# Kernel optimization log

Measured on AMD Instinct MI355X. Metric: run time of the kernel, lower is better.

## Reference

```python
import jax, jax.numpy as jnp
import numpy as np

IN_DIM, UNITS, OUT_DIM = 128, 256, 8
DENSITY = 0.5  # 1 - sparsity_level
B, T = 256, 512


def _ncp_dims():
    Nm = OUT_DIM
    Nc = max(int(0.4 * (UNITS - Nm)), 1)   # command neurons (AutoNCP rule)
    Ni = UNITS - Nm - Nc                    # inter neurons
    return Ni, Nc, Nm


def _fanout_mask(rng, n_src, n_dst, fanout):
    # each source connects to `fanout` distinct random destinations
    idx = np.argsort(rng.random((n_src, n_dst)), axis=1)[:, :fanout]
    m = np.zeros((n_src, n_dst), dtype=np.int32)
    m[np.arange(n_src)[:, None], idx] = 1
    return m


def setup_inputs() -> dict:
    key = jax.random.key(0)
    rng = np.random.default_rng(22222)
    Ni, Nc, Nm = _ncp_dims()
    s_fan = max(int(Ni * DENSITY), 1)       # sensory fanout
    i_fan = max(int(Nc * DENSITY), 1)       # inter fanout
    m_fanin = max(int(Nc * DENSITY), 1)     # motor fanin
    M_si = _fanout_mask(rng, IN_DIM, Ni, s_fan)      # sensory -> inter
    M_ic = _fanout_mask(rng, Ni, Nc, i_fan)          # inter -> command
    M_cm = _fanout_mask(rng, Nm, Nc, m_fanin).T      # command -> motor (fanin per motor)

    def layer_mask(M_in, hid):
        # WiredCfCCell: concat input sparsity with dense ones for the recurrent block, then transpose
        return np.concatenate([M_in, np.ones((hid, hid), np.int32)], axis=0).T

    masks = [layer_mask(M_si, Ni), layer_mask(M_ic, Nc), layer_mask(M_cm, Nm)]
    dims = [(IN_DIM, Ni), (Ni, Nc), (Nc, Nm)]
    inp = {}
    for l, (fin, hid) in enumerate(dims):
        cat = fin + hid
        scale = 1.0 / np.sqrt(cat)
        for nm in ("w1", "w2", "wa", "wb"):
            inp[f"{nm}_{l}"] = jnp.asarray(rng.normal(0.0, scale, (hid, cat)).astype(np.float32))
        for nm in ("b1", "b2", "ba", "bb"):
            inp[f"{nm}_{l}"] = jnp.zeros((hid,), jnp.float32)
        inp[f"m{l}"] = jnp.asarray(masks[l])  # int32, constant sparsity mask
    k1, k2 = jax.random.split(key)
    inp["x"] = jax.random.normal(k1, (B, T, IN_DIM), jnp.float32)
    inp["dt"] = jax.random.uniform(k2, (1,), jnp.float32, 0.5, 1.5)
    return inp


def _cfc_cell(xh, w1, b1, w2, b2, wa, ba, wb, bb, m, ts):
    # CfCCell, mode='default', no backbone, sparsity mask on ff1/ff2 weights
    mf = m.astype(w1.dtype)
    ff1 = jnp.tanh(xh @ (w1 * mf).T + b1)
    ff2 = jnp.tanh(xh @ (w2 * mf).T + b2)
    t_interp = jax.nn.sigmoid((xh @ wa.T + ba) * ts + (xh @ wb.T + bb))
    return ff1 * (1.0 - t_interp) + t_interp * ff2


def _forward(x, dt, params, masks):
    Ni, Nc, Nm = _ncp_dims()
    ts = dt[0]
    h0 = jnp.zeros((x.shape[0], Ni), x.dtype)
    h1 = jnp.zeros((x.shape[0], Nc), x.dtype)
    h2 = jnp.zeros((x.shape[0], Nm), x.dtype)
    p0, p1, p2 = params

    def step(carry, xt):
        h0, h1, h2 = carry
        nh0 = _cfc_cell(jnp.concatenate([xt, h0], 1), *p0, masks[0], ts)
        nh1 = _cfc_cell(jnp.concatenate([nh0, h1], 1), *p1, masks[1], ts)
        nh2 = _cfc_cell(jnp.concatenate([nh1, h2], 1), *p2, masks[2], ts)
        return (nh0, nh1, nh2), nh2

    (h0, h1, h2), ys = jax.lax.scan(step, (h0, h1, h2), jnp.swapaxes(x, 0, 1))
    y = jnp.tanh(jnp.swapaxes(ys, 0, 1))          # (B, T, OUT_DIM), tanh output saturation
    h_out = jnp.concatenate([h0, h1, h2], axis=1)  # (B, units)
    return y, h_out


def reference(x, dt,
              w1_0, b1_0, w2_0, b2_0, wa_0, ba_0, wb_0, bb_0, m0,
              w1_1, b1_1, w2_1, b2_1, wa_1, ba_1, wb_1, bb_1, m1,
              w1_2, b1_2, w2_2, b2_2, wa_2, ba_2, wb_2, bb_2, m2):
    params = ((w1_0, b1_0, w2_0, b2_0, wa_0, ba_0, wb_0, bb_0),
              (w1_1, b1_1, w2_1, b2_1, wa_1, ba_1, wb_1, bb_1),
              (w1_2, b1_2, w2_2, b2_2, wa_2, ba_2, wb_2, bb_2))
    return _forward(x, dt, params, (m0, m1, m2))
```

## Files before the change

### kernel.cpp

```cpp
#include <hip/hip_runtime.h>
#include <cmath>


typedef _Float16 f16;
typedef f16 h4 __attribute__((ext_vector_type(4)));
typedef f16 h8 __attribute__((ext_vector_type(8)));
typedef float f4 __attribute__((ext_vector_type(4)));

#define MFMA(a, b, c) __builtin_amdgcn_mfma_f32_16x16x32_f16(a, b, c, 0, 0, 0)
#define RAW_BAR() asm volatile("s_waitcnt lgkmcnt(0)\n\ts_barrier" ::: "memory")

constexpr int IN_DIM = 128, Ni = 149, Nc = 99, Nm = 8;
constexpr int CAT0 = 277, CAT1 = 248, CAT2 = 107;
constexpr int Bsz = 256, Tsz = 512;
constexpr int TC = 128, NCH = 4, NBT = 16;
constexpr int NT0 = 30, NT1 = 21;
constexpr int S0 = 168, S2 = 136;
constexpr size_t XU0_HALVES = (size_t)TC * NBT * NT0 * 256;
constexpr size_t NH0_HALVES = (size_t)TC * NBT * 16 * 160;
constexpr size_t XU1_HALVES = (size_t)TC * NBT * NT1 * 256;
constexpr size_t H0S_HALVES = (size_t)NBT * 16 * S0;
constexpr size_t H12S_HALVES = (size_t)NBT * 2 * 16 * S2;
constexpr size_t YOFF = (size_t)Bsz * Tsz * 8;

constexpr int OFF_X0 = 0;
constexpr int OFF_R0 = 7680;
constexpr int OFF_X1 = 17280;
constexpr int OFF_R12A = 24000;
constexpr int OFF_R12B = 29376;
constexpr int NFRAG = 30144;

__device__ inline float rcpf_(float x) { return __builtin_amdgcn_rcpf(x); }
__device__ __forceinline__ float cfc_h(float a0, float a1, float a2) {
  float e0 = __expf(a0), e1 = __expf(a1), e2 = __expf(a2);
  float pa = 1.f + e0, ma = 1.f - e0;
  float pb = 1.f + e1, mb = 1.f - e1;
  float pc = 1.f + e2;
  float num = fmaf(ma * pb, e2, mb * pa);
  return num * rcpf_(pa * pb * pc);
}
__device__ __forceinline__ float tanhp_(float x) {
  float e = __expf(-2.f * x);
  return (1.f - e) * rcpf_(1.f + e);
}

__global__ __launch_bounds__(256) void pack_kernel(
    const float* __restrict__ w1_0, const float* __restrict__ w2_0,
    const float* __restrict__ wa_0, const float* __restrict__ wb_0,
    const int* __restrict__ m0,
    const float* __restrict__ w1_1, const float* __restrict__ w2_1,
    const float* __restrict__ wa_1, const float* __restrict__ wb_1,
    const int* __restrict__ m1,
    const float* __restrict__ w1_2, const float* __restrict__ w2_2,
    const float* __restrict__ wa_2, const float* __restrict__ wb_2,
    const int* __restrict__ m2, const float* __restrict__ dtp,
    f16* __restrict__ PK) {
  int idx = blockIdx.x * 256 + threadIdx.x;
  if (idx >= NFRAG) return;
  int lane = idx & 63, col = lane & 15, q = lane >> 4;
  float ts = dtp[0];
  const float* Wa = nullptr;
  const float* Wb = nullptr;
  const int* M = nullptr;
  int ld, n, nmax, k0, kmax;
  int mat;
  if (idx < OFF_R0) {
    int p = idx >> 6;
    mat = p / 40; int nt = (p >> 2) % 10, kt = p & 3;
    ld = CAT0; n = nt * 16 + col; nmax = Ni; k0 = kt * 32 + q * 8; kmax = IN_DIM;
    if (mat == 0) { Wa = w1_0; M = m0; }
    else if (mat == 1) { Wa = w2_0; M = m0; }
    else { Wa = wa_0; Wb = wb_0; }
  } else if (idx < OFF_X1) {
    int p = (idx - OFF_R0) >> 6;
    int g = p / 15; mat = (p / 5) % 3; int kt = p % 5;
    ld = CAT0; n = g * 16 + col; nmax = Ni; k0 = IN_DIM + kt * 32 + q * 8; kmax = CAT0;
    if (mat == 0) Wa = w1_0;
    else if (mat == 1) Wa = w2_0;
    else { Wa = wa_0; Wb = wb_0; }
  } else if (idx < OFF_R12A) {
    int p = (idx - OFF_X1) >> 6;
    mat = p / 35; int nt = (p / 5) % 7, kt = p % 5;
    ld = CAT1; n = nt * 16 + col; nmax = Nc; k0 = kt * 32 + q * 8; kmax = Ni;
    if (mat == 0) { Wa = w1_1; M = m1; }
    else if (mat == 1) { Wa = w2_1; M = m1; }
    else { Wa = wa_1; Wb = wb_1; }
  } else if (idx < OFF_R12B) {
    int p = (idx - OFF_R12A) >> 6;
    int wv = p / 12; mat = (p / 4) % 3; int kt = p & 3;
    ld = CAT1; n = wv * 16 + col; nmax = Nc; k0 = Ni + kt * 32 + q * 8; kmax = CAT1;
    if (mat == 0) Wa = w1_1;
    else if (mat == 1) Wa = w2_1;
    else { Wa = wa_1; Wb = wb_1; }
  } else {
    int p = (idx - OFF_R12B) >> 6;
    mat = p / 4; int kt = p & 3;
    ld = CAT2; n = col; nmax = Nm; k0 = kt * 32 + q * 8; kmax = CAT2;
    if (mat == 0) { Wa = w1_2; M = m2; }
    else if (mat == 1) { Wa = w2_2; M = m2; }
    else { Wa = wa_2; Wb = wb_2; }
  }
  h8 r;
#pragma unroll
  for (int j = 0; j < 8; j++) {
    int k = k0 + j;
    float v = 0.f;
    if (n < nmax && k < kmax) {
      if (mat < 2) {
        v = Wa[(size_t)n * ld + k];
        if (M) v *= (float)M[(size_t)n * ld + k];
        v *= -2.f;
      } else {
        v = -(ts * Wa[(size_t)n * ld + k] + Wb[(size_t)n * ld + k]);
      }
    }
    r[j] = (f16)v;
  }
  ((h8*)PK)[idx] = r;
}

__global__ __launch_bounds__(192, 2) void X_kernel(
    const h8* __restrict__ pk, const float* __restrict__ x,
    const f16* __restrict__ NH0, f16* __restrict__ XU0, f16* __restrict__ XU1,
    const float* __restrict__ b1_0, const float* __restrict__ b2_0,
    const float* __restrict__ ba_0, const float* __restrict__ bb_0,
    const float* __restrict__ b1_1, const float* __restrict__ b2_1,
    const float* __restrict__ ba_1, const float* __restrict__ bb_1,
    const float* __restrict__ dtp, int c) {
  __shared__ f16 stg[16 * 136];
  int tid = threadIdx.x;
  int w = tid >> 6, lane = tid & 63, col = lane & 15, q = lane >> 4;
  int wg = blockIdx.x;
  float ts = dtp[0];
  if (wg < 512) {
    if (c < 0) return;
    h8 Bf[7][5];
    float bias[7];
#pragma unroll
    for (int nt = 0; nt < 7; nt++) {
#pragma unroll
      for (int kt = 0; kt < 5; kt++)
        Bf[nt][kt] = pk[OFF_X1 + ((w * 7 + nt) * 5 + kt) * 64 + lane];
      int n = nt * 16 + col;
      bias[nt] = (n < Nc) ? (w == 0 ? -2.f * b1_1[n]
                                    : (w == 1 ? -2.f * b2_1[n]
                                              : -(ts * ba_1[n] + bb_1[n])))
                          : 0.f;
    }
    for (int i = 0; i < 4; i++) {
      int mt = wg * 4 + i;
      const f16* Ab = NH0 + (size_t)mt * 2560;
      h8 A[5];
#pragma unroll
      for (int kt = 0; kt < 5; kt++)
        A[kt] = *(const h8*)(Ab + col * 160 + kt * 32 + q * 8);
#pragma unroll
      for (int nt = 0; nt < 7; nt++) {
        float b = bias[nt];
        f4 acc = {b, b, b, b};
#pragma unroll
        for (int kt = 0; kt < 5; kt++) acc = MFMA(A[kt], Bf[nt][kt], acc);
        h4 o;
#pragma unroll
        for (int rr = 0; rr < 4; rr++) o[rr] = (f16)acc[rr];
        *(h4*)(XU1 + ((size_t)mt * NT1 + w * 7 + nt) * 256 + lane * 4) = o;
      }
    }
  } else {
    int cn = c + 1;
    if (cn >= NCH) return;
    int bx = wg - 512;
    h8 Bf[10][4];
    float bias[10];
#pragma unroll
    for (int nt = 0; nt < 10; nt++) {
#pragma unroll
      for (int kt = 0; kt < 4; kt++)
        Bf[nt][kt] = pk[OFF_X0 + ((w * 10 + nt) * 4 + kt) * 64 + lane];
      int n = nt * 16 + col;
      bias[nt] = (n < Ni) ? (w == 0 ? -2.f * b1_0[n]
                                    : (w == 1 ? -2.f * b2_0[n]
                                              : -(ts * ba_0[n] + bb_0[n])))
                          : 0.f;
    }
    for (int i = 0; i < 4; i++) {
      int mt = bx * 4 + i;
      int tl = mt >> 4, bt = mt & 15;
      int tg = cn * TC + tl;
      if (tid < 128) {
        int sr = tid >> 3, sc = (tid & 7) * 16;
        const float* xp = x + ((size_t)(bt * 16 + sr) * Tsz + tg) * IN_DIM + sc;
        h8 hv0, hv1;
#pragma unroll
        for (int j = 0; j < 8; j++) hv0[j] = (f16)xp[j];
#pragma unroll
        for (int j = 0; j < 8; j++) hv1[j] = (f16)xp[8 + j];
        *(h8*)(stg + sr * 136 + sc) = hv0;
        *(h8*)(stg + sr * 136 + sc + 8) = hv1;
      }
      __syncthreads();
      h8 A[4];
#pragma unroll
      for (int kt = 0; kt < 4; kt++)
        A[kt] = *(const h8*)(stg + col * 136 + kt * 32 + q * 8);
#pragma unroll
      for (int nt = 0; nt < 10; nt++) {
        float b = bias[nt];
        f4 acc = {b, b, b, b};
#pragma unroll
        for (int kt = 0; kt < 4; kt++) acc = MFMA(A[kt], Bf[nt][kt], acc);
        h4 o;
#pragma unroll
        for (int rr = 0; rr < 4; rr++) o[rr] = (f16)acc[rr];
        *(h4*)(XU0 + ((size_t)mt * NT0 + w * 10 + nt) * 256 + lane * 4) = o;
      }
      __syncthreads();
    }
  }
}

__device__ __forceinline__ void r0_step(
    const f16* br, f16* bw, const f16* __restrict__ XU0, f16* __restrict__ NH0,
    float* __restrict__ out, const h8 (&Bf)[3][5], h4 (&xu)[3],
    int t, int tload, int bt, int g, int lane, int col, int q, int n, bool last) {
  h8 A[5];
#pragma unroll
  for (int kt = 0; kt < 5; kt++)
    A[kt] = *(const h8*)(br + col * S0 + kt * 32 + q * 8);
  f4 acc0 = {(float)xu[0][0], (float)xu[0][1], (float)xu[0][2], (float)xu[0][3]};
  f4 acc1 = {(float)xu[1][0], (float)xu[1][1], (float)xu[1][2], (float)xu[1][3]};
  f4 acc2 = {(float)xu[2][0], (float)xu[2][1], (float)xu[2][2], (float)xu[2][3]};
  size_t mtl = (size_t)tload * NBT + bt;
#pragma unroll
  for (int mat = 0; mat < 3; mat++)
    xu[mat] = *(const h4*)(XU0 + (mtl * NT0 + mat * 10 + g) * 256 + lane * 4);
#pragma unroll
  for (int kt = 0; kt < 5; kt++) {
    acc0 = MFMA(A[kt], Bf[0][kt], acc0);
    acc1 = MFMA(A[kt], Bf[1][kt], acc1);
    acc2 = MFMA(A[kt], Bf[2][kt], acc2);
  }
  int mt = t * NBT + bt;
  f16* nh = NH0 + (size_t)mt * 2560;
#pragma unroll
  for (int r = 0; r < 4; r++) {
    int m = q * 4 + r;
    float h = cfc_h(acc0[r], acc1[r], acc2[r]);
    f16 h16 = (f16)h;
    bw[m * S0 + n] = h16;
    nh[m * 160 + n] = h16;
    if (last && n < Ni) out[YOFF + (size_t)(bt * 16 + m) * 256 + n] = h;
  }
}

__device__ __forceinline__ void r12l1_step(
    const f16* br, f16* bw, const f16* __restrict__ XU1, float* __restrict__ out,
    const h8 (&Bf)[3][4], h4 (&xu)[3],
    int tload, int bt, int w, int lane, int col, int q, int n, bool last) {
  h8 A[4];
#pragma unroll
  for (int kt = 0; kt < 4; kt++)
    A[kt] = *(const h8*)(br + col * S2 + kt * 32 + q * 8);
  f4 acc0 = {(float)xu[0][0], (float)xu[0][1], (float)xu[0][2], (float)xu[0][3]};
  f4 acc1 = {(float)xu[1][0], (float)xu[1][1], (float)xu[1][2], (float)xu[1][3]};
  f4 acc2 = {(float)xu[2][0], (float)xu[2][1], (float)xu[2][2], (float)xu[2][3]};
  size_t mtl = (size_t)tload * NBT + bt;
#pragma unroll
  for (int mat = 0; mat < 3; mat++)
    xu[mat] = *(const h4*)(XU1 + (mtl * NT1 + mat * 7 + w) * 256 + lane * 4);
#pragma unroll
  for (int kt = 0; kt < 4; kt++) {
    acc0 = MFMA(A[kt], Bf[0][kt], acc0);
    acc1 = MFMA(A[kt], Bf[1][kt], acc1);
    acc2 = MFMA(A[kt], Bf[2][kt], acc2);
  }
#pragma unroll
  for (int r = 0; r < 4; r++) {
    int m = q * 4 + r;
    float h = cfc_h(acc0[r], acc1[r], acc2[r]);
    if (n < Nc) {
      bw[m * S2 + n] = (f16)h;
      if (last) out[YOFF + (size_t)(bt * 16 + m) * 256 + Ni + n] = h;
    }
  }
}

__device__ __forceinline__ void r12l2_step(
    const f16* rb, f16* wb, float* __restrict__ out, const h8 (&Bf)[3][4],
    float bn0, float bn1, float bn2, int tg, int bt, int col, int q, bool last) {
  h8 A[4];
#pragma unroll
  for (int kt = 0; kt < 4; kt++)
    A[kt] = *(const h8*)(rb + col * S2 + kt * 32 + q * 8);
  f4 acc0 = {bn0, bn0, bn0, bn0};
  f4 acc1 = {bn1, bn1, bn1, bn1};
  f4 acc2 = {bn2, bn2, bn2, bn2};
#pragma unroll
  for (int kt = 0; kt < 4; kt++) {
    acc0 = MFMA(A[kt], Bf[0][kt], acc0);
    acc1 = MFMA(A[kt], Bf[1][kt], acc1);
    acc2 = MFMA(A[kt], Bf[2][kt], acc2);
  }
#pragma unroll
  for (int r = 0; r < 4; r++) {
    int m = q * 4 + r;
    float h = cfc_h(acc0[r], acc1[r], acc2[r]);
    if (col < Nm) {
      out[((size_t)(bt * 16 + m) * Tsz + tg) * 8 + col] = tanhp_(h);
      wb[m * S2 + Nc + col] = (f16)h;
      if (last) out[YOFF + (size_t)(bt * 16 + m) * 256 + Ni + Nc + col] = h;
    }
  }
}

__global__ __launch_bounds__(640) void R_kernel(
    const h8* __restrict__ pk,
    const float* __restrict__ c1, const float* __restrict__ c2,
    const float* __restrict__ ca, const float* __restrict__ cb,
    const float* __restrict__ dtp, const f16* __restrict__ XU0,
    const f16* __restrict__ XU1, f16* __restrict__ NH0,
    f16* __restrict__ H0S, f16* __restrict__ H12S, float* __restrict__ out, int c) {
  __shared__ __align__(16) char smem[2 * 16 * S0 * 2];
  int tid = threadIdx.x;
  int g = tid >> 6, lane = tid & 63, col = lane & 15, q = lane >> 4;
  int wg = blockIdx.x;

  if (wg < NBT) {
    if (c >= NCH) return;
    f16(*buf)[16 * S0] = (f16(*)[16 * S0])smem;
    int bt = wg;
    int n = g * 16 + col;
    h8 Bf[3][5];
#pragma unroll
    for (int mat = 0; mat < 3; mat++)
#pragma unroll
      for (int kt = 0; kt < 5; kt++)
        Bf[mat][kt] = pk[OFF_R0 + ((g * 3 + mat) * 5 + kt) * 64 + lane];

    for (int idx = tid; idx < 16 * S0; idx += 640) {
      buf[0][idx] = (c == 0) ? (f16)0.f : H0S[(size_t)bt * 16 * S0 + idx];
      buf[1][idx] = (f16)0.f;
    }
    __syncthreads();

    h4 xuA[3], xuB[3];
#pragma unroll
    for (int mat = 0; mat < 3; mat++) {
      xuA[mat] = *(const h4*)(XU0 + ((size_t)bt * NT0 + mat * 10 + g) * 256 + lane * 4);
      xuB[mat] =
          *(const h4*)(XU0 + ((size_t)(NBT + bt) * NT0 + mat * 10 + g) * 256 + lane * 4);
    }

    for (int t = 0; t < TC; t += 2) {
      bool lastA = (c == NCH - 1) && (t == TC - 1);
      int tlA = (t + 2 < TC) ? t + 2 : t;
      r0_step(buf[0], buf[1], XU0, NH0, out, Bf, xuA, t, tlA, bt, g, lane, col, q, n,
              lastA);
      RAW_BAR();
      bool lastB = (c == NCH - 1) && (t + 1 == TC - 1);
      int tlB = (t + 3 < TC) ? t + 3 : t + 1;
      r0_step(buf[1], buf[0], XU0, NH0, out, Bf, xuB, t + 1, tlB, bt, g, lane, col, q,
              n, lastB);
      RAW_BAR();
    }
    for (int idx = tid; idx < 16 * S0; idx += 640)
      H0S[(size_t)bt * 16 * S0 + idx] = buf[0][idx];

  } else {
    int cc = c - 1;
    if (cc < 0) return;
    f16(*buf)[16 * S2] = (f16(*)[16 * S2])smem;
    int bt = wg - NBT;
    int w = g;
    float ts = dtp[0];
    h8 Bf[3][4];
    float bn0 = 0.f, bn1 = 0.f, bn2 = 0.f;
    int n = w * 16 + col;
    if (w < 7) {
#pragma unroll
      for (int mat = 0; mat < 3; mat++)
#pragma unroll
        for (int kt = 0; kt < 4; kt++)
          Bf[mat][kt] = pk[OFF_R12A + ((w * 3 + mat) * 4 + kt) * 64 + lane];
    } else if (w == 7) {
#pragma unroll
      for (int mat = 0; mat < 3; mat++)
#pragma unroll
        for (int kt = 0; kt < 4; kt++)
          Bf[mat][kt] = pk[OFF_R12B + (mat * 4 + kt) * 64 + lane];
      bn0 = (col < Nm) ? -2.f * c1[col] : 0.f;
      bn1 = (col < Nm) ? -2.f * c2[col] : 0.f;
      bn2 = (col < Nm) ? -(ts * ca[col] + cb[col]) : 0.f;
    }
    for (int idx = tid; idx < 2 * 16 * S2; idx += 640)
      ((f16*)buf)[idx] = (cc == 0) ? (f16)0.f : H12S[(size_t)bt * 2 * 16 * S2 + idx];
    __syncthreads();

    h4 xuA[3], xuB[3];
    if (w < 7) {
#pragma unroll
      for (int mat = 0; mat < 3; mat++) {
        xuA[mat] =
            *(const h4*)(XU1 + ((size_t)bt * NT1 + mat * 7 + w) * 256 + lane * 4);
        xuB[mat] = *(const h4*)(XU1 +
                                ((size_t)(NBT + bt) * NT1 + mat * 7 + w) * 256 +
                                lane * 4);
      }
    }

    for (int t = 0; t < TC; t += 2) {
      if (w < 7) {
        int tlA = (t + 2 < TC) ? t + 2 : t;
        bool lastA = (cc == NCH - 1) && (t == TC - 1);
        r12l1_step(buf[0], buf[1], XU1, out, Bf, xuA, tlA, bt, w, lane, col, q, n,
                   lastA);
      }
      RAW_BAR();
      if (w == 7)
        r12l2_step(buf[1], buf[0], out, Bf, bn0, bn1, bn2, cc * TC + t, bt, col, q,
                   false);
      if (w < 7) {
        int tlB = (t + 3 < TC) ? t + 3 : t + 1;
        bool lastB = (cc == NCH - 1) && (t + 1 == TC - 1);
        r12l1_step(buf[1], buf[0], XU1, out, Bf, xuB, tlB, bt, w, lane, col, q, n,
                   lastB);
      }
      RAW_BAR();
      if (w == 7)
        r12l2_step(buf[0], buf[1], out, Bf, bn0, bn1, bn2, cc * TC + t + 1, bt, col, q,
                   (cc == NCH - 1) && (t + 1 == TC - 1));
    }
    __syncthreads();
    for (int idx = tid; idx < 2 * 16 * S2; idx += 640)
      H12S[(size_t)bt * 2 * 16 * S2 + idx] = ((f16*)buf)[idx];
  }
}

extern "C" void kernel_launch(void* const* d_in, const int* in_sizes, int n_in,
                              void* d_out, int out_size, void* d_ws, size_t ws_size,
                              hipStream_t stream) {
  const float* w1_0 = (const float*)d_in[0];
  const float* w2_0 = (const float*)d_in[1];
  const float* wa_0 = (const float*)d_in[2];
  const float* wb_0 = (const float*)d_in[3];
  const float* b1_0 = (const float*)d_in[4];
  const float* b2_0 = (const float*)d_in[5];
  const float* ba_0 = (const float*)d_in[6];
  const float* bb_0 = (const float*)d_in[7];
  const int* m0 = (const int*)d_in[8];
  const float* w1_1 = (const float*)d_in[9];
  const float* w2_1 = (const float*)d_in[10];
  const float* wa_1 = (const float*)d_in[11];
  const float* wb_1 = (const float*)d_in[12];
  const float* b1_1 = (const float*)d_in[13];
  const float* b2_1 = (const float*)d_in[14];
  const float* ba_1 = (const float*)d_in[15];
  const float* bb_1 = (const float*)d_in[16];
  const int* m1 = (const int*)d_in[17];
  const float* w1_2 = (const float*)d_in[18];
  const float* w2_2 = (const float*)d_in[19];
  const float* wa_2 = (const float*)d_in[20];
  const float* wb_2 = (const float*)d_in[21];
  const float* c1 = (const float*)d_in[22];
  const float* c2 = (const float*)d_in[23];
  const float* ca = (const float*)d_in[24];
  const float* cb = (const float*)d_in[25];
  const int* m2 = (const int*)d_in[26];
  const float* x = (const float*)d_in[27];
  const float* dt = (const float*)d_in[28];
  float* out = (float*)d_out;

  f16* XU0 = (f16*)d_ws;
  f16* NH0 = XU0 + XU0_HALVES;
  f16* XU1 = NH0 + NH0_HALVES;
  f16* H0S = XU1 + XU1_HALVES;
  f16* H12S = H0S + H0S_HALVES;
  f16* PK = H12S + H12S_HALVES;
  const h8* pk = (const h8*)PK;

  pack_kernel<<<(NFRAG + 255) / 256, 256, 0, stream>>>(
      w1_0, w2_0, wa_0, wb_0, m0, w1_1, w2_1, wa_1, wb_1, m1,
      w1_2, w2_2, wa_2, wb_2, m2, dt, PK);

  X_kernel<<<1024, 192, 0, stream>>>(pk, x, NH0, XU0, XU1, b1_0, b2_0, ba_0, bb_0,
                                     b1_1, b2_1, ba_1, bb_1, dt, -1);

  for (int c = 0; c <= NCH; c++) {
    R_kernel<<<32, 640, 0, stream>>>(pk, c1, c2, ca, cb, dt, XU0, XU1, NH0, H0S,
                                     H12S, out, c);
    if (c < NCH)
      X_kernel<<<1024, 192, 0, stream>>>(pk, x, NH0, XU0, XU1, b1_0, b2_0, ba_0,
                                         bb_0, b1_1, b2_1, ba_1, bb_1, dt, c);
  }
}
```

Measured before the change: 826.9 us.

## Process two batch tiles per recurrent workgroup to interleave independent MFMA chains

Each recurrent workgroup now handles two 16-row batch tiles at once, with the step functions computing both tiles' MFMA chains and CfC activations interleaved. The R_kernel grid drops from 32 to 16 blocks and shared memory doubles. The goal is to hide MFMA and LDS latency on the serial time-step chain with independent work from the second tile, and to halve the barrier count per tile. In exchange each step does roughly twice the work on fewer CUs, which lengthens per-step critical-path latency and raises register pressure.

Result: slower. 1.330 ms (+60.8%).

```diff
diff --git a/kernel.cpp b/kernel.cpp
--- a/kernel.cpp
+++ b/kernel.cpp
@@ -22,6 +22,8 @@
 constexpr size_t H0S_HALVES = (size_t)NBT * 16 * S0;
 constexpr size_t H12S_HALVES = (size_t)NBT * 2 * 16 * S2;
 constexpr size_t YOFF = (size_t)Bsz * Tsz * 8;
+constexpr size_t STR0 = (size_t)NBT * NT0 * 256;
+constexpr size_t STR1 = (size_t)NBT * NT1 * 256;
 
 constexpr int OFF_X0 = 0;
 constexpr int OFF_R0 = 7680;
@@ -219,96 +221,139 @@
   }
 }
 
-__device__ __forceinline__ void r0_step(
-    const f16* br, f16* bw, const f16* __restrict__ XU0, f16* __restrict__ NH0,
-    float* __restrict__ out, const h8 (&Bf)[3][5], h4 (&xu)[3],
-    int t, int tload, int bt, int g, int lane, int col, int q, int n, bool last) {
-  h8 A[5];
-#pragma unroll
-  for (int kt = 0; kt < 5; kt++)
-    A[kt] = *(const h8*)(br + col * S0 + kt * 32 + q * 8);
-  f4 acc0 = {(float)xu[0][0], (float)xu[0][1], (float)xu[0][2], (float)xu[0][3]};
-  f4 acc1 = {(float)xu[1][0], (float)xu[1][1], (float)xu[1][2], (float)xu[1][3]};
-  f4 acc2 = {(float)xu[2][0], (float)xu[2][1], (float)xu[2][2], (float)xu[2][3]};
-  size_t mtl = (size_t)tload * NBT + bt;
-#pragma unroll
-  for (int mat = 0; mat < 3; mat++)
-    xu[mat] = *(const h4*)(XU0 + (mtl * NT0 + mat * 10 + g) * 256 + lane * 4);
+__device__ __forceinline__ void r0_step2(
+    const f16* br0, const f16* br1, f16* bw0, f16* bw1,
+    const f16* const (&xb0)[3], const f16* const (&xb1)[3], int tload,
+    const h8 (&Bf)[3][5], h4 (&xu0)[3], h4 (&xu1)[3],
+    f16* __restrict__ NH0, float* __restrict__ out,
+    int t, int bt0, int bt1, int q, int col, int n, bool last) {
+  h8 A0[5], A1[5];
 #pragma unroll
   for (int kt = 0; kt < 5; kt++) {
-    acc0 = MFMA(A[kt], Bf[0][kt], acc0);
-    acc1 = MFMA(A[kt], Bf[1][kt], acc1);
-    acc2 = MFMA(A[kt], Bf[2][kt], acc2);
-  }
-  int mt = t * NBT + bt;
-  f16* nh = NH0 + (size_t)mt * 2560;
+    A0[kt] = *(const h8*)(br0 + col * S0 + kt * 32 + q * 8);
+    A1[kt] = *(const h8*)(br1 + col * S0 + kt * 32 + q * 8);
+  }
+  f4 a00 = {(float)xu0[0][0], (float)xu0[0][1], (float)xu0[0][2], (float)xu0[0][3]};
+  f4 a01 = {(float)xu0[1][0], (float)xu0[1][1], (float)xu0[1][2], (float)xu0[1][3]};
+  f4 a02 = {(float)xu0[2][0], (float)xu0[2][1], (float)xu0[2][2], (float)xu0[2][3]};
+  f4 a10 = {(float)xu1[0][0], (float)xu1[0][1], (float)xu1[0][2], (float)xu1[0][3]};
+  f4 a11 = {(float)xu1[1][0], (float)xu1[1][1], (float)xu1[1][2], (float)xu1[1][3]};
+  f4 a12 = {(float)xu1[2][0], (float)xu1[2][1], (float)xu1[2][2], (float)xu1[2][3]};
+#pragma unroll
+  for (int mat = 0; mat < 3; mat++) {
+    xu0[mat] = *(const h4*)(xb0[mat] + (size_t)tload * STR0);
+    xu1[mat] = *(const h4*)(xb1[mat] + (size_t)tload * STR0);
+  }
+#pragma unroll
+  for (int kt = 0; kt < 5; kt++) {
+    a00 = MFMA(A0[kt], Bf[0][kt], a00);
+    a01 = MFMA(A0[kt], Bf[1][kt], a01);
+    a02 = MFMA(A0[kt], Bf[2][kt], a02);
+    a10 = MFMA(A1[kt], Bf[0][kt], a10);
+    a11 = MFMA(A1[kt], Bf[1][kt], a11);
+    a12 = MFMA(A1[kt], Bf[2][kt], a12);
+  }
+  f16* nh0 = NH0 + ((size_t)t * NBT + bt0) * 2560;
+  f16* nh1 = NH0 + ((size_t)t * NBT + bt1) * 2560;
 #pragma unroll
   for (int r = 0; r < 4; r++) {
     int m = q * 4 + r;
-    float h = cfc_h(acc0[r], acc1[r], acc2[r]);
-    f16 h16 = (f16)h;
-    bw[m * S0 + n] = h16;
-    nh[m * 160 + n] = h16;
-    if (last && n < Ni) out[YOFF + (size_t)(bt * 16 + m) * 256 + n] = h;
-  }
-}
-
-__device__ __forceinline__ void r12l1_step(
-    const f16* br, f16* bw, const f16* __restrict__ XU1, float* __restrict__ out,
-    const h8 (&Bf)[3][4], h4 (&xu)[3],
-    int tload, int bt, int w, int lane, int col, int q, int n, bool last) {
-  h8 A[4];
-#pragma unroll
-  for (int kt = 0; kt < 4; kt++)
-    A[kt] = *(const h8*)(br + col * S2 + kt * 32 + q * 8);
-  f4 acc0 = {(float)xu[0][0], (float)xu[0][1], (float)xu[0][2], (float)xu[0][3]};
-  f4 acc1 = {(float)xu[1][0], (float)xu[1][1], (float)xu[1][2], (float)xu[1][3]};
-  f4 acc2 = {(float)xu[2][0], (float)xu[2][1], (float)xu[2][2], (float)xu[2][3]};
-  size_t mtl = (size_t)tload * NBT + bt;
-#pragma unroll
-  for (int mat = 0; mat < 3; mat++)
-    xu[mat] = *(const h4*)(XU1 + (mtl * NT1 + mat * 7 + w) * 256 + lane * 4);
+    float h0 = cfc_h(a00[r], a01[r], a02[r]);
+    float h1 = cfc_h(a10[r], a11[r], a12[r]);
+    f16 g0 = (f16)h0, g1 = (f16)h1;
+    bw0[m * S0 + n] = g0;
+    bw1[m * S0 + n] = g1;
+    nh0[m * 160 + n] = g0;
+    nh1[m * 160 + n] = g1;
+    if (last && n < Ni) {
+      out[YOFF + (size_t)(bt0 * 16 + m) * 256 + n] = h0;
+      out[YOFF + (size_t)(bt1 * 16 + m) * 256 + n] = h1;
+    }
+  }
+}
+
+__device__ __forceinline__ void r12l1_step2(
+    const f16* br0, const f16* br1, f16* bw0, f16* bw1,
+    const f16* const (&xb0)[3], const f16* const (&xb1)[3], int tload,
+    const h8 (&Bf)[3][4], h4 (&xu0)[3], h4 (&xu1)[3],
+    float* __restrict__ out, int bt0, int bt1, int q, int col, int n, bool last) {
+  h8 A0[4], A1[4];
 #pragma unroll
   for (int kt = 0; kt < 4; kt++) {
-    acc0 = MFMA(A[kt], Bf[0][kt], acc0);
-    acc1 = MFMA(A[kt], Bf[1][kt], acc1);
-    acc2 = MFMA(A[kt], Bf[2][kt], acc2);
+    A0[kt] = *(const h8*)(br0 + col * S2 + kt * 32 + q * 8);
+    A1[kt] = *(const h8*)(br1 + col * S2 + kt * 32 + q * 8);
+  }
+  f4 a00 = {(float)xu0[0][0], (float)xu0[0][1], (float)xu0[0][2], (float)xu0[0][3]};
+  f4 a01 = {(float)xu0[1][0], (float)xu0[1][1], (float)xu0[1][2], (float)xu0[1][3]};
+  f4 a02 = {(float)xu0[2][0], (float)xu0[2][1], (float)xu0[2][2], (float)xu0[2][3]};
+  f4 a10 = {(float)xu1[0][0], (float)xu1[0][1], (float)xu1[0][2], (float)xu1[0][3]};
+  f4 a11 = {(float)xu1[1][0], (float)xu1[1][1], (float)xu1[1][2], (float)xu1[1][3]};
+  f4 a12 = {(float)xu1[2][0], (float)xu1[2][1], (float)xu1[2][2], (float)xu1[2][3]};
+#pragma unroll
+  for (int mat = 0; mat < 3; mat++) {
+    xu0[mat] = *(const h4*)(xb0[mat] + (size_t)tload * STR1);
+    xu1[mat] = *(const h4*)(xb1[mat] + (size_t)tload * STR1);
+  }
+#pragma unroll
+  for (int kt = 0; kt < 4; kt++) {
+    a00 = MFMA(A0[kt], Bf[0][kt], a00);
+    a01 = MFMA(A0[kt], Bf[1][kt], a01);
+    a02 = MFMA(A0[kt], Bf[2][kt], a02);
+    a10 = MFMA(A1[kt], Bf[0][kt], a10);
+    a11 = MFMA(A1[kt], Bf[1][kt], a11);
+    a12 = MFMA(A1[kt], Bf[2][kt], a12);
   }
 #pragma unroll
   for (int r = 0; r < 4; r++) {
     int m = q * 4 + r;
-    float h = cfc_h(acc0[r], acc1[r], acc2[r]);
+    float h0 = cfc_h(a00[r], a01[r], a02[r]);
+    float h1 = cfc_h(a10[r], a11[r], a12[r]);
     if (n < Nc) {
-      bw[m * S2 + n] = (f16)h;
-      if (last) out[YOFF + (size_t)(bt * 16 + m) * 256 + Ni + n] = h;
-    }
-  }
-}
-
-__device__ __forceinline__ void r12l2_step(
-    const f16* rb, f16* wb, float* __restrict__ out, const h8 (&Bf)[3][4],
-    float bn0, float bn1, float bn2, int tg, int bt, int col, int q, bool last) {
-  h8 A[4];
-#pragma unroll
-  for (int kt = 0; kt < 4; kt++)
-    A[kt] = *(const h8*)(rb + col * S2 + kt * 32 + q * 8);
-  f4 acc0 = {bn0, bn0, bn0, bn0};
-  f4 acc1 = {bn1, bn1, bn1, bn1};
-  f4 acc2 = {bn2, bn2, bn2, bn2};
+      bw0[m * S2 + n] = (f16)h0;
+      bw1[m * S2 + n] = (f16)h1;
+      if (last) {
+        out[YOFF + (size_t)(bt0 * 16 + m) * 256 + Ni + n] = h0;
+        out[YOFF + (size_t)(bt1 * 16 + m) * 256 + Ni + n] = h1;
+      }
+    }
+  }
+}
+
+__device__ __forceinline__ void r12l2_step2(
+    const f16* rb0, const f16* rb1, f16* wb0, f16* wb1, float* __restrict__ out,
+    const h8 (&Bf)[3][4], float bn0, float bn1, float bn2, int tg, int bt0, int bt1,
+    int col, int q, bool last) {
+  h8 A0[4], A1[4];
 #pragma unroll
   for (int kt = 0; kt < 4; kt++) {
-    acc0 = MFMA(A[kt], Bf[0][kt], acc0);
-    acc1 = MFMA(A[kt], Bf[1][kt], acc1);
-    acc2 = MFMA(A[kt], Bf[2][kt], acc2);
+    A0[kt] = *(const h8*)(rb0 + col * S2 + kt * 32 + q * 8);
+    A1[kt] = *(const h8*)(rb1 + col * S2 + kt * 32 + q * 8);
+  }
+  f4 a00 = {bn0, bn0, bn0, bn0}, a01 = {bn1, bn1, bn1, bn1}, a02 = {bn2, bn2, bn2, bn2};
+  f4 a10 = a00, a11 = a01, a12 = a02;
+#pragma unroll
+  for (int kt = 0; kt < 4; kt++) {
+    a00 = MFMA(A0[kt], Bf[0][kt], a00);
+    a01 = MFMA(A0[kt], Bf[1][kt], a01);
+    a02 = MFMA(A0[kt], Bf[2][kt], a02);
+    a10 = MFMA(A1[kt], Bf[0][kt], a10);
+    a11 = MFMA(A1[kt], Bf[1][kt], a11);
+    a12 = MFMA(A1[kt], Bf[2][kt], a12);
   }
 #pragma unroll
   for (int r = 0; r < 4; r++) {
     int m = q * 4 + r;
-    float h = cfc_h(acc0[r], acc1[r], acc2[r]);
+    float h0 = cfc_h(a00[r], a01[r], a02[r]);
+    float h1 = cfc_h(a10[r], a11[r], a12[r]);
     if (col < Nm) {
-      out[((size_t)(bt * 16 + m) * Tsz + tg) * 8 + col] = tanhp_(h);
-      wb[m * S2 + Nc + col] = (f16)h;
-      if (last) out[YOFF + (size_t)(bt * 16 + m) * 256 + Ni + Nc + col] = h;
+      out[((size_t)(bt0 * 16 + m) * Tsz + tg) * 8 + col] = tanhp_(h0);
+      out[((size_t)(bt1 * 16 + m) * Tsz + tg) * 8 + col] = tanhp_(h1);
+      wb0[m * S2 + Nc + col] = (f16)h0;
+      wb1[m * S2 + Nc + col] = (f16)h1;
+      if (last) {
+        out[YOFF + (size_t)(bt0 * 16 + m) * 256 + Ni + Nc + col] = h0;
+        out[YOFF + (size_t)(bt1 * 16 + m) * 256 + Ni + Nc + col] = h1;
+      }
     }
   }
 }
@@ -320,15 +365,17 @@
     const float* __restrict__ dtp, const f16* __restrict__ XU0,
     const f16* __restrict__ XU1, f16* __restrict__ NH0,
     f16* __restrict__ H0S, f16* __restrict__ H12S, float* __restrict__ out, int c) {
-  __shared__ __align__(16) char smem[2 * 16 * S0 * 2];
+  __shared__ __align__(16) char smem[2 * 2 * 16 * S0 * 2];
   int tid = threadIdx.x;
   int g = tid >> 6, lane = tid & 63, col = lane & 15, q = lane >> 4;
   int wg = blockIdx.x;
 
-  if (wg < NBT) {
+  if (wg < 8) {
     if (c >= NCH) return;
-    f16(*buf)[16 * S0] = (f16(*)[16 * S0])smem;
-    int bt = wg;
+    typedef f16 (*BufT)[16 * S0];
+    BufT B0 = (BufT)smem;
+    BufT B1 = (BufT)(smem + 2 * 16 * S0 * 2);
+    int bt0 = 2 * wg, bt1 = 2 * wg + 1;
     int n = g * 16 + col;
     h8 Bf[3][5];
 #pragma unroll
@@ -337,51 +384,69 @@
       for (int kt = 0; kt < 5; kt++)
         Bf[mat][kt] = pk[OFF_R0 + ((g * 3 + mat) * 5 + kt) * 64 + lane];
 
+    const f16* xb0[3];
+    const f16* xb1[3];
+#pragma unroll
+    for (int mat = 0; mat < 3; mat++) {
+      xb0[mat] = XU0 + ((size_t)bt0 * NT0 + mat * 10 + g) * 256 + lane * 4;
+      xb1[mat] = XU0 + ((size_t)bt1 * NT0 + mat * 10 + g) * 256 + lane * 4;
+    }
     for (int idx = tid; idx < 16 * S0; idx += 640) {
-      buf[0][idx] = (c == 0) ? (f16)0.f : H0S[(size_t)bt * 16 * S0 + idx];
-      buf[1][idx] = (f16)0.f;
+      B0[0][idx] = (c == 0) ? (f16)0.f : H0S[(size_t)bt0 * 16 * S0 + idx];
+      B1[0][idx] = (c == 0) ? (f16)0.f : H0S[(size_t)bt1 * 16 * S0 + idx];
+      B0[1][idx] = (f16)0.f;
+      B1[1][idx] = (f16)0.f;
     }
     __syncthreads();
 
-    h4 xuA[3], xuB[3];
+    h4 xuA0[3], xuA1[3], xuB0[3], xuB1[3];
 #pragma unroll
     for (int mat = 0; mat < 3; mat++) {
-      xuA[mat] = *(const h4*)(XU0 + ((size_t)bt * NT0 + mat * 10 + g) * 256 + lane * 4);
-      xuB[mat] =
-          *(const h4*)(XU0 + ((size_t)(NBT + bt) * NT0 + mat * 10 + g) * 256 + lane * 4);
+      xuA0[mat] = *(const h4*)(xb0[mat]);
+      xuA1[mat] = *(const h4*)(xb1[mat]);
+      xuB0[mat] = *(const h4*)(xb0[mat] + STR0);
+      xuB1[mat] = *(const h4*)(xb1[mat] + STR0);
     }
 
     for (int t = 0; t < TC; t += 2) {
-      bool lastA = (c == NCH - 1) && (t == TC - 1);
-      int tlA = (t + 2 < TC) ? t + 2 : t;
-      r0_step(buf[0], buf[1], XU0, NH0, out, Bf, xuA, t, tlA, bt, g, lane, col, q, n,
-              lastA);
+      int tlA = (t + 2 < TC) ? t + 2 : TC - 1;
+      r0_step2(B0[0], B1[0], B0[1], B1[1], xb0, xb1, tlA, Bf, xuA0, xuA1, NH0, out,
+               t, bt0, bt1, q, col, n, false);
       RAW_BAR();
+      int tlB = (t + 3 < TC) ? t + 3 : TC - 1;
       bool lastB = (c == NCH - 1) && (t + 1 == TC - 1);
-      int tlB = (t + 3 < TC) ? t + 3 : t + 1;
-      r0_step(buf[1], buf[0], XU0, NH0, out, Bf, xuB, t + 1, tlB, bt, g, lane, col, q,
-              n, lastB);
+      r0_step2(B0[1], B1[1], B0[0], B1[0], xb0, xb1, tlB, Bf, xuB0, xuB1, NH0, out,
+               t + 1, bt0, bt1, q, col, n, lastB);
       RAW_BAR();
     }
-    for (int idx = tid; idx < 16 * S0; idx += 640)
-      H0S[(size_t)bt * 16 * S0 + idx] = buf[0][idx];
+    for (int idx = tid; idx < 16 * S0; idx += 640) {
+      H0S[(size_t)bt0 * 16 * S0 + idx] = B0[0][idx];
+      H0S[(size_t)bt1 * 16 * S0 + idx] = B1[0][idx];
+    }
 
   } else {
     int cc = c - 1;
     if (cc < 0) return;
-    f16(*buf)[16 * S2] = (f16(*)[16 * S2])smem;
-    int bt = wg - NBT;
+    typedef f16 (*BufT)[16 * S2];
+    BufT B0 = (BufT)smem;
+    BufT B1 = (BufT)(smem + 2 * 16 * S2 * 2);
+    int bt0 = 2 * (wg - 8), bt1 = bt0 + 1;
     int w = g;
     float ts = dtp[0];
     h8 Bf[3][4];
     float bn0 = 0.f, bn1 = 0.f, bn2 = 0.f;
     int n = w * 16 + col;
+    const f16* xb0[3] = {XU1, XU1, XU1};
+    const f16* xb1[3] = {XU1, XU1, XU1};
     if (w < 7) {
 #pragma unroll
-      for (int mat = 0; mat < 3; mat++)
+      for (int mat = 0; mat < 3; mat++) {
 #pragma unroll
         for (int kt = 0; kt < 4; kt++)
           Bf[mat][kt] = pk[OFF_R12A + ((w * 3 + mat) * 4 + kt) * 64 + lane];
+        xb0[mat] = XU1 + ((size_t)bt0 * NT1 + mat * 7 + w) * 256 + lane * 4;
+        xb1[mat] = XU1 + ((size_t)bt1 * NT1 + mat * 7 + w) * 256 + lane * 4;
+      }
     } else if (w == 7) {
 #pragma unroll
       for (int mat = 0; mat < 3; mat++)
@@ -392,47 +457,49 @@
       bn1 = (col < Nm) ? -2.f * c2[col] : 0.f;
       bn2 = (col < Nm) ? -(ts * ca[col] + cb[col]) : 0.f;
     }
-    for (int idx = tid; idx < 2 * 16 * S2; idx += 640)
-      ((f16*)buf)[idx] = (cc == 0) ? (f16)0.f : H12S[(size_t)bt * 2 * 16 * S2 + idx];
+    for (int idx = tid; idx < 2 * 16 * S2; idx += 640) {
+      ((f16*)B0)[idx] = (cc == 0) ? (f16)0.f : H12S[(size_t)bt0 * 2 * 16 * S2 + idx];
+      ((f16*)B1)[idx] = (cc == 0) ? (f16)0.f : H12S[(size_t)bt1 * 2 * 16 * S2 + idx];
+    }
     __syncthreads();
 
-    h4 xuA[3], xuB[3];
+    h4 xuA0[3], xuA1[3], xuB0[3], xuB1[3];
     if (w < 7) {
 #pragma unroll
       for (int mat = 0; mat < 3; mat++) {
-        xuA[mat] =
-            *(const h4*)(XU1 + ((size_t)bt * NT1 + mat * 7 + w) * 256 + lane * 4);
-        xuB[mat] = *(const h4*)(XU1 +
-                                ((size_t)(NBT + bt) * NT1 + mat * 7 + w) * 256 +
-                                lane * 4);
-      }
-    }
-
+        xuA0[mat] = *(const h4*)(xb0[mat]);
+        xuA1[mat] = *(const h4*)(xb1[mat]);
+        xuB0[mat] = *(const h4*)(xb0[mat] + STR1);
+        xuB1[mat] = *(const h4*)(xb1[mat] + STR1);
+      }
+    }
     for (int t = 0; t < TC; t += 2) {
       if (w < 7) {
-        int tlA = (t + 2 < TC) ? t + 2 : t;
-        bool lastA = (cc == NCH - 1) && (t == TC - 1);
-        r12l1_step(buf[0], buf[1], XU1, out, Bf, xuA, tlA, bt, w, lane, col, q, n,
-                   lastA);
+        int tlA = (t + 2 < TC) ? t + 2 : TC - 1;
+        r12l1_step2(B0[0], B1[0], B0[1], B1[1], xb0, xb1, tlA, Bf, xuA0, xuA1, out,
+                    bt0, bt1, q, col, n, false);
       }
       RAW_BAR();
       if (w == 7)
-        r12l2_step(buf[1], buf[0], out, Bf, bn0, bn1, bn2, cc * TC + t, bt, col, q,
-                   false);
+        r12l2_step2(B0[1], B1[1], B0[0], B1[0], out, Bf, bn0, bn1, bn2, cc * TC + t,
+                    bt0, bt1, col, q, false);
       if (w < 7) {
-        int tlB = (t + 3 < TC) ? t + 3 : t + 1;
+        int tlB = (t + 3 < TC) ? t + 3 : TC - 1;
         bool lastB = (cc == NCH - 1) && (t + 1 == TC - 1);
-        r12l1_step(buf[1], buf[0], XU1, out, Bf, xuB, tlB, bt, w, lane, col, q, n,
-                   lastB);
+        r12l1_step2(B0[1], B1[1], B0[0], B1[0], xb0, xb1, tlB, Bf, xuB0, xuB1, out,
+                    bt0, bt1, q, col, n, lastB);
       }
       RAW_BAR();
       if (w == 7)
-        r12l2_step(buf[0], buf[1], out, Bf, bn0, bn1, bn2, cc * TC + t + 1, bt, col, q,
-                   (cc == NCH - 1) && (t + 1 == TC - 1));
+        r12l2_step2(B0[0], B1[0], B0[1], B1[1], out, Bf, bn0, bn1, bn2,
+                    cc * TC + t + 1, bt0, bt1, col, q,
+                    (cc == NCH - 1) && (t + 1 == TC - 1));
     }
     __syncthreads();
-    for (int idx = tid; idx < 2 * 16 * S2; idx += 640)
-      H12S[(size_t)bt * 2 * 16 * S2 + idx] = ((f16*)buf)[idx];
+    for (int idx = tid; idx < 2 * 16 * S2; idx += 640) {
+      H12S[(size_t)bt0 * 2 * 16 * S2 + idx] = ((f16*)B0)[idx];
+      H12S[(size_t)bt1 * 2 * 16 * S2 + idx] = ((f16*)B1)[idx];
+    }
   }
 }
 
@@ -486,7 +553,7 @@
                                      b1_1, b2_1, ba_1, bb_1, dt, -1);
 
   for (int c = 0; c <= NCH; c++) {
-    R_kernel<<<32, 640, 0, stream>>>(pk, c1, c2, ca, cb, dt, XU0, XU1, NH0, H0S,
+    R_kernel<<<16, 640, 0, stream>>>(pk, c1, c2, ca, cb, dt, XU0, XU1, NH0, H0S,
                                      H12S, out, c);
     if (c < NCH)
       X_kernel<<<1024, 192, 0, stream>>>(pk, x, NH0, XU0, XU1, b1_0, b2_0, ba_0,
```
